# Kernel tuning notes

Measured on AMD Instinct MI355X. Metric: run time of the kernel, lower is better.

## Reference

```python
import jax, jax.numpy as jnp
import numpy as np

N_NODES = 50000
N_EDGES = 400000
IN_DIM = 256
HID = 64
HEADS = 8
OUT_DIM = 256
NEG_SLOPE = 0.2


def setup_inputs() -> dict:
    key = jax.random.key(0)
    ks = jax.random.split(key, 6)
    x = jax.random.normal(ks[0], (N_NODES, IN_DIM), dtype=jnp.float32)
    edge_index = jax.random.randint(ks[1], (2, N_EDGES), 0, N_NODES, dtype=jnp.int64)
    # per-head W: [H, in, hid]; per-head attention vector a: [H, 2*hid]
    W = jax.random.normal(ks[2], (HEADS, IN_DIM, HID), dtype=jnp.float32) * (1.0 / np.sqrt(IN_DIM))
    a = jax.random.normal(ks[3], (HEADS, 2 * HID), dtype=jnp.float32) * (1.0 / np.sqrt(2 * HID))
    Wo = jax.random.normal(ks[4], (HEADS * HID, OUT_DIM), dtype=jnp.float32) * (1.0 / np.sqrt(HEADS * HID))
    bo = jnp.zeros((OUT_DIM,), dtype=jnp.float32)
    return {"x": x, "edge_index": edge_index, "W": W, "a": a, "Wo": Wo, "bo": bo}


def _gat_forward(x, edge_index, W, a, Wo, bo):
    n = x.shape[0]
    src, tgt = edge_index[0], edge_index[1]
    # per-head projections: [N, H, hid]
    h = jnp.einsum('ni,hio->nho', x, W)
    # split attention vector: score(e) = a1.h_src + a2.h_tgt (cat-then-dot decomposed)
    a_src, a_tgt = a[:, :HID], a[:, HID:]
    s_src = jnp.einsum('nho,ho->nh', h, a_src)  # [N, H]
    s_tgt = jnp.einsum('nho,ho->nh', h, a_tgt)  # [N, H]
    e = s_src[src] + s_tgt[tgt]                  # [E, H]
    e = jnp.where(e >= 0, e, NEG_SLOPE * e)      # leaky_relu(0.2)
    # segment softmax keyed on target node (PyG-style)
    m = jax.ops.segment_max(e, tgt, num_segments=n)          # [N, H]
    ex = jnp.exp(e - m[tgt])                                  # [E, H]
    denom = jax.ops.segment_sum(ex, tgt, num_segments=n)     # [N, H]
    alpha = ex / (denom[tgt] + 1e-16)                          # [E, H]
    # weighted scatter-add of source features: [N, H, hid]
    msgs = h[src] * alpha[:, :, None]
    out = jax.ops.segment_sum(msgs, tgt, num_segments=n)
    out = out.reshape(n, HEADS * HID)
    out = out @ Wo + bo
    return jax.nn.elu(out)


def reference(x, edge_index, W, a, Wo, bo):
    return _gat_forward(x, edge_index, W, a, Wo, bo)
```

## Files before the change

kernel.cpp:

```cpp
#include <hip/hip_runtime.h>
#include <hip/hip_bf16.h>
#include <math.h>

#define N_NODES 50000
#define N_EDGES 400000
#define IN_DIM 256
#define HID 64
#define HEADS 8
#define OUT_DIM 256
#define NEG_SLOPE 0.2f
#define BUCKET 64

#define CVTW_BLOCKS 512
#define CVTWO_BLOCKS 512
#define FILL_BLOCKS 1563

#define SEG_BLOCKS 1024
#define SEG_WAVES (SEG_BLOCKS * 4)

typedef __attribute__((ext_vector_type(8))) short bf16x8;
typedef __attribute__((ext_vector_type(4))) float f32x4;

static __device__ __forceinline__ unsigned short f2bf(float f) {
    unsigned int u = __float_as_uint(f);
    unsigned int r = (u + 0x7fffu + ((u >> 16) & 1u)) >> 16;
    return (unsigned short)r;
}
static __device__ __forceinline__ float bf2f(unsigned short s) {
    return __uint_as_float((unsigned int)s << 16);
}
static __device__ __forceinline__ bf16x8 cvt8(const float* __restrict__ p) {
    bf16x8 r;
    #pragma unroll
    for (int j = 0; j < 8; ++j) r[j] = (short)f2bf(p[j]);
    return r;
}

__global__ __launch_bounds__(256) void prep_kernel(
    const float* __restrict__ W, unsigned short* __restrict__ Wt,
    const float* __restrict__ Wo, unsigned short* __restrict__ Wot,
    const int* __restrict__ ei, int* __restrict__ deg,
    int* __restrict__ csr)
{
    const int b = blockIdx.x;
    if (b < CVTW_BLOCKS) {
        const int i = b * 256 + threadIdx.x;
        const int hd = i >> 14;
        const int o  = (i >> 8) & 63;
        const int k  = i & 255;
        Wt[i] = f2bf(W[((size_t)hd * IN_DIM + k) * HID + o]);
    } else if (b < CVTW_BLOCKS + CVTWO_BLOCKS) {
        const int i = (b - CVTW_BLOCKS) * 256 + threadIdx.x;
        const int n = i >> 9;
        const int k = i & 511;
        Wot[i] = f2bf(Wo[(size_t)k * OUT_DIM + n]);
    } else {
        const int e = (b - CVTW_BLOCKS - CVTWO_BLOCKS) * 256 + threadIdx.x;
        if (e < N_EDGES) {
            const int src = ei[e];
            const int tgt = ei[N_EDGES + e];
            const int pos = atomicAdd(&deg[tgt], 1);
            if (pos < BUCKET) csr[tgt * BUCKET + pos] = src;
        }
    }
}

template<int K, int LDC, int EPI, int CVTA>
__global__ __launch_bounds__(512) void gemm_mfma(
    const void* __restrict__ Av,
    const unsigned short* __restrict__ Bt,
    const float* __restrict__ bias,
    void* __restrict__ Cv)
{
    const int m0 = blockIdx.x * 128;
    const int n0 = blockIdx.y * 256;
    const int tid = threadIdx.x;
    const int lane = tid & 63;
    const int w = tid >> 6;
    const int wr = w >> 2;
    const int wn = w & 3;
    __shared__ unsigned short lA[128 * 64];
    __shared__ unsigned short lB[256 * 64];

    const int ca0 = tid,       ra0 = ca0 >> 3, ga0 = ca0 & 7;
    const int ca1 = tid + 512, ra1 = ca1 >> 3, ga1 = ca1 & 7;
    const int ua0 = (((ra0 >> 4) * 8 + ga0) * 16) + (ra0 & 15);
    const int ua1 = (((ra1 >> 4) * 8 + ga1) * 16) + (ra1 & 15);
    int am0 = m0 + ra0; if (am0 >= N_NODES) am0 = N_NODES - 1;
    int am1 = m0 + ra1; if (am1 >= N_NODES) am1 = N_NODES - 1;
    const float* Af0 = nullptr; const float* Af1 = nullptr;
    const unsigned short* Ab0 = nullptr; const unsigned short* Ab1 = nullptr;
    if constexpr (CVTA) {
        const float* Af = (const float*)Av;
        Af0 = Af + (size_t)am0 * K + ga0 * 8;
        Af1 = Af + (size_t)am1 * K + ga1 * 8;
    } else {
        const unsigned short* Ab = (const unsigned short*)Av;
        Ab0 = Ab + (size_t)am0 * K + ga0 * 8;
        Ab1 = Ab + (size_t)am1 * K + ga1 * 8;
    }

    const unsigned short* Bp[4];
    int ub[4];
    #pragma unroll
    for (int j = 0; j < 4; ++j) {
        const int cb = tid + j * 512;
        const int rb = cb >> 3, gb = cb & 7;
        ub[j] = (((rb >> 4) * 8 + gb) * 16) + (rb & 15);
        Bp[j] = Bt + (size_t)(n0 + rb) * K + gb * 8;
    }

    f32x4 acc[4][4];
    #pragma unroll
    for (int t = 0; t < 4; ++t)
        #pragma unroll
        for (int n = 0; n < 4; ++n) acc[t][n] = (f32x4){0,0,0,0};

    for (int k0 = 0; k0 < K; k0 += 64) {
        if constexpr (CVTA) {
            *(bf16x8*)(lA + ua0 * 8) = cvt8(Af0 + k0);
            *(bf16x8*)(lA + ua1 * 8) = cvt8(Af1 + k0);
        } else {
            *(bf16x8*)(lA + ua0 * 8) = *(const bf16x8*)(Ab0 + k0);
            *(bf16x8*)(lA + ua1 * 8) = *(const bf16x8*)(Ab1 + k0);
        }
        #pragma unroll
        for (int j = 0; j < 4; ++j)
            *(bf16x8*)(lB + ub[j] * 8) = *(const bf16x8*)(Bp[j] + k0);
        __syncthreads();
        #pragma unroll
        for (int kk = 0; kk < 2; ++kk) {
            bf16x8 bfr[4];
            #pragma unroll
            for (int n = 0; n < 4; ++n)
                bfr[n] = *(const bf16x8*)(lB + ((wn * 4 + n) * 128 + kk * 64 + lane) * 8);
            #pragma unroll
            for (int t = 0; t < 4; ++t) {
                const bf16x8 afr = *(const bf16x8*)(lA + ((wr * 4 + t) * 128 + kk * 64 + lane) * 8);
                #pragma unroll
                for (int n = 0; n < 4; ++n)
                    acc[t][n] = __builtin_amdgcn_mfma_f32_16x16x32_bf16(afr, bfr[n], acc[t][n], 0, 0, 0);
            }
        }
        __syncthreads();
    }

    #pragma unroll
    for (int n = 0; n < 4; ++n) {
        const int col = n0 + wn * 64 + n * 16 + (lane & 15);
        float b = 0.0f;
        if (EPI == 1) b = bias[col];
        #pragma unroll
        for (int t = 0; t < 4; ++t) {
            #pragma unroll
            for (int r = 0; r < 4; ++r) {
                const int m = m0 + wr * 64 + t * 16 + ((lane >> 4) << 2) + r;
                if (m < N_NODES) {
                    const float v = acc[t][n][r];
                    if (EPI == 0) {
                        ((unsigned short*)Cv)[(size_t)m * LDC + col] = f2bf(v);
                    } else {
                        float z = v + b;
                        ((float*)Cv)[(size_t)m * LDC + col] = (z > 0.0f) ? z : expm1f(z);
                    }
                }
            }
        }
    }
}

__global__ __launch_bounds__(256) void s_kernel(
    const unsigned short* __restrict__ hb, const float* __restrict__ a,
    float* __restrict__ s_src, float* __restrict__ s_tgt)
{
    const int n = blockIdx.x * 4 + (threadIdx.x >> 6);
    const int lane = threadIdx.x & 63;
    if (n >= N_NODES) return;
    const int hd = lane >> 3;
    const int seg = lane & 7;
    const bf16x8 hv = *(const bf16x8*)(hb + (size_t)n * 512 + lane * 8);
    float p = 0.0f, q = 0.0f;
    #pragma unroll
    for (int j = 0; j < 8; ++j) {
        const float hf = bf2f((unsigned short)hv[j]);
        p = fmaf(hf, a[hd * 128 + seg * 8 + j], p);
        q = fmaf(hf, a[hd * 128 + 64 + seg * 8 + j], q);
    }
    #pragma unroll
    for (int off = 1; off < 8; off <<= 1) {
        p += __shfl_xor(p, off);
        q += __shfl_xor(q, off);
    }
    if (seg == 0) {
        s_src[(size_t)n * 8 + hd] = p;
        s_tgt[(size_t)n * 8 + hd] = q;
    }
}

__global__ __launch_bounds__(256) void segment_kernel(
    const int* __restrict__ deg, const int* __restrict__ csr,
    const float* __restrict__ s_src, const float* __restrict__ s_tgt,
    const unsigned short* __restrict__ hb, unsigned short* __restrict__ accb)
{
    const int gw = blockIdx.x * 4 + (threadIdx.x >> 6);
    const int lane = threadIdx.x & 63;
    const int myhead = lane >> 3;
    const int islot = lane >> 3;
    const int pj = lane & 7;

    for (int t = gw; t < N_NODES; t += SEG_WAVES) {
        const int cnt = min(deg[t], BUCKET);
        const float st = s_tgt[(size_t)t * 8 + pj];

        float dsum = 0.0f;
        float msg[8] = {};
        int my_src = 0;
        if (lane < cnt) my_src = csr[t * BUCKET + lane];
        for (int b = 0; b * 8 < cnt; ++b) {
            const int nb = min(8, cnt - b * 8);
            const int esrc = __shfl(my_src, b * 8 + islot);
            float pv = 0.0f;
            if (islot < nb) {
                float v = s_src[(size_t)esrc * 8 + pj] + st;
                v = (v >= 0.0f) ? v : NEG_SLOPE * v;
                pv = expf(v);
            }
            dsum += pv;
            int i = 0;
            for (; i + 4 <= nb; i += 4) {
                int  sr[4]; float al[4]; bf16x8 hv[4];
                #pragma unroll
                for (int u = 0; u < 4; ++u) {
                    sr[u] = __shfl(my_src, b * 8 + i + u);
                    al[u] = __shfl(pv, (i + u) * 8 + myhead);
                }
                #pragma unroll
                for (int u = 0; u < 4; ++u)
                    hv[u] = *(const bf16x8*)(hb + (size_t)sr[u] * 512 + lane * 8);
                #pragma unroll
                for (int u = 0; u < 4; ++u)
                    #pragma unroll
                    for (int j = 0; j < 8; ++j)
                        msg[j] = fmaf(bf2f((unsigned short)hv[u][j]), al[u], msg[j]);
            }
            for (; i < nb; ++i) {
                const int src = __shfl(my_src, b * 8 + i);
                const float al = __shfl(pv, i * 8 + myhead);
                const bf16x8 hv = *(const bf16x8*)(hb + (size_t)src * 512 + lane * 8);
                #pragma unroll
                for (int j = 0; j < 8; ++j)
                    msg[j] = fmaf(bf2f((unsigned short)hv[j]), al, msg[j]);
            }
        }
        dsum += __shfl_xor(dsum, 8);
        dsum += __shfl_xor(dsum, 16);
        dsum += __shfl_xor(dsum, 32);
        const float d = __shfl(dsum, myhead) + 1e-16f;
        bf16x8 ov;
        #pragma unroll
        for (int j = 0; j < 8; ++j) ov[j] = (short)f2bf(msg[j] / d);
        *(bf16x8*)(accb + (size_t)t * 512 + lane * 8) = ov;
    }
}

extern "C" void kernel_launch(void* const* d_in, const int* in_sizes, int n_in,
                              void* d_out, int out_size, void* d_ws, size_t ws_size,
                              hipStream_t stream) {
    const float* x   = (const float*)d_in[0];
    const int*   ei  = (const int*)d_in[1];
    const float* W   = (const float*)d_in[2];
    const float* a   = (const float*)d_in[3];
    const float* Wo  = (const float*)d_in[4];
    const float* bo  = (const float*)d_in[5];
    float* out = (float*)d_out;

    unsigned short* hb   = (unsigned short*)d_ws;
    const size_t hsz = (size_t)N_NODES * HEADS * HID;
    unsigned short* accb = hb + hsz;
    unsigned short* Wt   = accb + hsz;
    unsigned short* Wot  = Wt + (size_t)HEADS * HID * IN_DIM;
    float* s_src = (float*)(Wot + (size_t)(HEADS * HID) * OUT_DIM);
    float* s_tgt = s_src + (size_t)N_NODES * HEADS;
    int* deg = (int*)(s_tgt + (size_t)N_NODES * HEADS);
    int* csr = deg + N_NODES;

    hipMemsetAsync(deg, 0, N_NODES * sizeof(int), stream);

    prep_kernel<<<CVTW_BLOCKS + CVTWO_BLOCKS + FILL_BLOCKS, 256, 0, stream>>>(
        W, Wt, Wo, Wot, ei, deg, csr);

    dim3 g1((N_NODES + 127) / 128, (HEADS * HID) / 256);
    gemm_mfma<IN_DIM, HEADS * HID, 0, 1><<<g1, 512, 0, stream>>>(
        x, Wt, nullptr, hb);

    s_kernel<<<(N_NODES + 3) / 4, 256, 0, stream>>>(hb, a, s_src, s_tgt);

    segment_kernel<<<SEG_BLOCKS, 256, 0, stream>>>(
        deg, csr, s_src, s_tgt, hb, accb);

    dim3 g5((N_NODES + 127) / 128, OUT_DIM / 256);
    gemm_mfma<HEADS * HID, OUT_DIM, 1, 0><<<g5, 512, 0, stream>>>(
        accb, Wot, bo, out);
}
```

Baseline: 205.2 us.

## Fuse attention score computation into segment aggregation kernel

Removes the separate s_kernel and its s_src/s_tgt buffers. The segment kernel now computes the target score from its own h row and each source score from the h row it already gathers for the message, using per-lane copies of the attention vector and xor-shuffle reductions. The launch also switches from a grid-stride loop over 1024 blocks to one wave per node. This saves a kernel launch and the score write/read traffic, at the cost of extra FMAs and shuffles per edge in the gather loop.

New measurement: 192.8 us. -6.0%, faster.

```diff
diff --git a/kernel.cpp b/kernel.cpp
--- a/kernel.cpp
+++ b/kernel.cpp
@@ -14,9 +14,6 @@
 #define CVTW_BLOCKS 512
 #define CVTWO_BLOCKS 512
 #define FILL_BLOCKS 1563
-
-#define SEG_BLOCKS 1024
-#define SEG_WAVES (SEG_BLOCKS * 4)
 
 typedef __attribute__((ext_vector_type(8))) short bf16x8;
 typedef __attribute__((ext_vector_type(4))) float f32x4;
@@ -169,98 +166,100 @@
     }
 }
 
-__global__ __launch_bounds__(256) void s_kernel(
-    const unsigned short* __restrict__ hb, const float* __restrict__ a,
-    float* __restrict__ s_src, float* __restrict__ s_tgt)
-{
-    const int n = blockIdx.x * 4 + (threadIdx.x >> 6);
-    const int lane = threadIdx.x & 63;
-    if (n >= N_NODES) return;
-    const int hd = lane >> 3;
-    const int seg = lane & 7;
-    const bf16x8 hv = *(const bf16x8*)(hb + (size_t)n * 512 + lane * 8);
-    float p = 0.0f, q = 0.0f;
-    #pragma unroll
-    for (int j = 0; j < 8; ++j) {
-        const float hf = bf2f((unsigned short)hv[j]);
-        p = fmaf(hf, a[hd * 128 + seg * 8 + j], p);
-        q = fmaf(hf, a[hd * 128 + 64 + seg * 8 + j], q);
-    }
-    #pragma unroll
-    for (int off = 1; off < 8; off <<= 1) {
-        p += __shfl_xor(p, off);
-        q += __shfl_xor(q, off);
-    }
-    if (seg == 0) {
-        s_src[(size_t)n * 8 + hd] = p;
-        s_tgt[(size_t)n * 8 + hd] = q;
-    }
-}
-
 __global__ __launch_bounds__(256) void segment_kernel(
     const int* __restrict__ deg, const int* __restrict__ csr,
-    const float* __restrict__ s_src, const float* __restrict__ s_tgt,
+    const float* __restrict__ a,
     const unsigned short* __restrict__ hb, unsigned short* __restrict__ accb)
 {
-    const int gw = blockIdx.x * 4 + (threadIdx.x >> 6);
+    const int t = blockIdx.x * 4 + (threadIdx.x >> 6);
     const int lane = threadIdx.x & 63;
+    if (t >= N_NODES) return;
     const int myhead = lane >> 3;
-    const int islot = lane >> 3;
-    const int pj = lane & 7;
-
-    for (int t = gw; t < N_NODES; t += SEG_WAVES) {
-        const int cnt = min(deg[t], BUCKET);
-        const float st = s_tgt[(size_t)t * 8 + pj];
-
-        float dsum = 0.0f;
-        float msg[8] = {};
-        int my_src = 0;
-        if (lane < cnt) my_src = csr[t * BUCKET + lane];
-        for (int b = 0; b * 8 < cnt; ++b) {
-            const int nb = min(8, cnt - b * 8);
-            const int esrc = __shfl(my_src, b * 8 + islot);
-            float pv = 0.0f;
-            if (islot < nb) {
-                float v = s_src[(size_t)esrc * 8 + pj] + st;
-                v = (v >= 0.0f) ? v : NEG_SLOPE * v;
-                pv = expf(v);
-            }
+    const int seg = lane & 7;
+
+    float ra[8], rq[8];
+    #pragma unroll
+    for (int j = 0; j < 8; ++j) {
+        ra[j] = a[myhead * 128 + seg * 8 + j];
+        rq[j] = a[myhead * 128 + 64 + seg * 8 + j];
+    }
+
+    float st;
+    {
+        const bf16x8 ht = *(const bf16x8*)(hb + (size_t)t * 512 + lane * 8);
+        float q = 0.0f;
+        #pragma unroll
+        for (int j = 0; j < 8; ++j)
+            q = fmaf(bf2f((unsigned short)ht[j]), rq[j], q);
+        q += __shfl_xor(q, 1);
+        q += __shfl_xor(q, 2);
+        q += __shfl_xor(q, 4);
+        st = q;
+    }
+
+    const int cnt = min(deg[t], BUCKET);
+    int my_src = 0;
+    if (lane < cnt) my_src = csr[t * BUCKET + lane];
+
+    float dsum = 0.0f;
+    float msg[8] = {};
+    int i = 0;
+    for (; i + 4 <= cnt; i += 4) {
+        int sr[4]; bf16x8 hv[4];
+        #pragma unroll
+        for (int u = 0; u < 4; ++u) sr[u] = __shfl(my_src, i + u);
+        #pragma unroll
+        for (int u = 0; u < 4; ++u)
+            hv[u] = *(const bf16x8*)(hb + (size_t)sr[u] * 512 + lane * 8);
+        float p[4];
+        #pragma unroll
+        for (int u = 0; u < 4; ++u) {
+            float s = 0.0f;
+            #pragma unroll
+            for (int j = 0; j < 8; ++j)
+                s = fmaf(bf2f((unsigned short)hv[u][j]), ra[j], s);
+            p[u] = s;
+        }
+        #pragma unroll
+        for (int u = 0; u < 4; ++u) {
+            p[u] += __shfl_xor(p[u], 1);
+            p[u] += __shfl_xor(p[u], 2);
+            p[u] += __shfl_xor(p[u], 4);
+        }
+        #pragma unroll
+        for (int u = 0; u < 4; ++u) {
+            float v = p[u] + st;
+            v = (v >= 0.0f) ? v : NEG_SLOPE * v;
+            const float pv = expf(v);
             dsum += pv;
-            int i = 0;
-            for (; i + 4 <= nb; i += 4) {
-                int  sr[4]; float al[4]; bf16x8 hv[4];
-                #pragma unroll
-                for (int u = 0; u < 4; ++u) {
-                    sr[u] = __shfl(my_src, b * 8 + i + u);
-                    al[u] = __shfl(pv, (i + u) * 8 + myhead);
-                }
-                #pragma unroll
-                for (int u = 0; u < 4; ++u)
-                    hv[u] = *(const bf16x8*)(hb + (size_t)sr[u] * 512 + lane * 8);
-                #pragma unroll
-                for (int u = 0; u < 4; ++u)
-                    #pragma unroll
-                    for (int j = 0; j < 8; ++j)
-                        msg[j] = fmaf(bf2f((unsigned short)hv[u][j]), al[u], msg[j]);
-            }
-            for (; i < nb; ++i) {
-                const int src = __shfl(my_src, b * 8 + i);
-                const float al = __shfl(pv, i * 8 + myhead);
-                const bf16x8 hv = *(const bf16x8*)(hb + (size_t)src * 512 + lane * 8);
-                #pragma unroll
-                for (int j = 0; j < 8; ++j)
-                    msg[j] = fmaf(bf2f((unsigned short)hv[j]), al, msg[j]);
-            }
-        }
-        dsum += __shfl_xor(dsum, 8);
-        dsum += __shfl_xor(dsum, 16);
-        dsum += __shfl_xor(dsum, 32);
-        const float d = __shfl(dsum, myhead) + 1e-16f;
-        bf16x8 ov;
-        #pragma unroll
-        for (int j = 0; j < 8; ++j) ov[j] = (short)f2bf(msg[j] / d);
-        *(bf16x8*)(accb + (size_t)t * 512 + lane * 8) = ov;
-    }
+            #pragma unroll
+            for (int j = 0; j < 8; ++j)
+                msg[j] = fmaf(bf2f((unsigned short)hv[u][j]), pv, msg[j]);
+        }
+    }
+    for (; i < cnt; ++i) {
+        const int src = __shfl(my_src, i);
+        const bf16x8 hv = *(const bf16x8*)(hb + (size_t)src * 512 + lane * 8);
+        float s = 0.0f;
+        #pragma unroll
+        for (int j = 0; j < 8; ++j)
+            s = fmaf(bf2f((unsigned short)hv[j]), ra[j], s);
+        s += __shfl_xor(s, 1);
+        s += __shfl_xor(s, 2);
+        s += __shfl_xor(s, 4);
+        float v = s + st;
+        v = (v >= 0.0f) ? v : NEG_SLOPE * v;
+        const float pv = expf(v);
+        dsum += pv;
+        #pragma unroll
+        for (int j = 0; j < 8; ++j)
+            msg[j] = fmaf(bf2f((unsigned short)hv[j]), pv, msg[j]);
+    }
+    const float d = dsum + 1e-16f;
+    bf16x8 ov;
+    #pragma unroll
+    for (int j = 0; j < 8; ++j) ov[j] = (short)f2bf(msg[j] / d);
+    *(bf16x8*)(accb + (size_t)t * 512 + lane * 8) = ov;
 }
 
 extern "C" void kernel_launch(void* const* d_in, const int* in_sizes, int n_in,
@@ -279,9 +278,7 @@
     unsigned short* accb = hb + hsz;
     unsigned short* Wt   = accb + hsz;
     unsigned short* Wot  = Wt + (size_t)HEADS * HID * IN_DIM;
-    float* s_src = (float*)(Wot + (size_t)(HEADS * HID) * OUT_DIM);
-    float* s_tgt = s_src + (size_t)N_NODES * HEADS;
-    int* deg = (int*)(s_tgt + (size_t)N_NODES * HEADS);
+    int* deg = (int*)(Wot + (size_t)(HEADS * HID) * OUT_DIM);
     int* csr = deg + N_NODES;
 
     hipMemsetAsync(deg, 0, N_NODES * sizeof(int), stream);
@@ -293,10 +290,8 @@
     gemm_mfma<IN_DIM, HEADS * HID, 0, 1><<<g1, 512, 0, stream>>>(
         x, Wt, nullptr, hb);
 
-    s_kernel<<<(N_NODES + 3) / 4, 256, 0, stream>>>(hb, a, s_src, s_tgt);
-
-    segment_kernel<<<SEG_BLOCKS, 256, 0, stream>>>(
-        deg, csr, s_src, s_tgt, hb, accb);
+    segment_kernel<<<(N_NODES + 3) / 4, 256, 0, stream>>>(
+        deg, csr, a, hb, accb);
 
     dim3 g5((N_NODES + 127) / 128, OUT_DIM / 256);
     gemm_mfma<HEADS * HID, OUT_DIM, 1, 0><<<g5, 512, 0, stream>>>(
```
